# Kernel optimization log

Hardware: AMD Instinct MI355X
Metric: run time of the kernel (lower is better)

Reference implementation:

```python
import jax, jax.numpy as jnp
import numpy as np

D = 512          # input_size (feature dim)
C = 100          # num_classes
N = 2048         # test samples
ALPHA = 0.5      # regularization mixing parameter
SHRINK = 1e-4    # shrinkage_param


def setup_inputs() -> dict:
    key = jax.random.key(0)
    k1, k2, k3, k4, k5 = jax.random.split(key, 5)
    X = jax.random.normal(k1, (N, D), dtype=jnp.float32)
    muK = jax.random.normal(k2, (C, D), dtype=jnp.float32)
    # Per-class covariances: PSD, well-conditioned (like fitted streaming covariances)
    A = jax.random.normal(k3, (C, D, D), dtype=jnp.float32) * 0.05
    SigmaK = jnp.einsum('cij,ckj->cik', A, A) + 0.1 * jnp.eye(D, dtype=jnp.float32)
    B = jax.random.normal(k4, (D, D), dtype=jnp.float32) * 0.05
    Sigma = B @ B.T + 0.1 * jnp.eye(D, dtype=jnp.float32)
    # class counts (all > 0 so every class is active)
    cK = jax.random.uniform(k5, (C,), dtype=jnp.float32, minval=1.0, maxval=1000.0)
    return {"X": X, "muK": muK, "SigmaK": SigmaK, "Sigma": Sigma, "cK": cK}


def reference(X, muK, SigmaK, Sigma, cK):
    # RegSigmaK[k] = alpha * SigmaK[k] + (1-alpha) * Sigma           [C, D, D]
    RegSigmaK = ALPHA * SigmaK + (1.0 - ALPHA) * Sigma[None, :, :]
    # priors (classes with zero count get prior 1, then are masked to -inf below)
    s = jnp.sum(cK)
    prior = jnp.where(cK == 0, 1.0, cK / s)                          # [C]
    # Lambda[k] = pinv((1-sh) * RegSigmaK[k] + sh * I)               [C, D, D]
    eye = jnp.eye(D, dtype=RegSigmaK.dtype)
    Lambda = jnp.linalg.pinv((1.0 - SHRINK) * RegSigmaK + SHRINK * eye)
    # 0.5 * log ||RegSigmaK[k]||_F  (torch.norm default = Frobenius)
    half_lognorm = 0.5 * jnp.log(jnp.linalg.norm(RegSigmaK, axis=(1, 2)))  # [C]
    # batched Mahalanobis quadratic form: (x - mu_k)^T Lambda_k (x - mu_k)
    diff = X[:, None, :] - muK[None, :, :]                           # [N, C, D]
    quad = jnp.einsum('ncd,cde,nce->nc', diff, Lambda, diff)         # [N, C]
    scores = jnp.log(prior)[None, :] - half_lognorm[None, :] - 0.5 * quad
    scores = jnp.where((cK == 0)[None, :], -jnp.inf, scores)
    return scores
```

## Files before the change

kernel.cpp:

```cpp
#include <hip/hip_runtime.h>
#include <math.h>

#define DIM 512
#define NCLS 100
#define NS 2048
#define DD (DIM*DIM)
#define SHRINKV 1e-4f

typedef short bf16x8 __attribute__((ext_vector_type(8)));
typedef short s16x4 __attribute__((ext_vector_type(4)));
typedef float f32x4 __attribute__((ext_vector_type(4)));

static __device__ __forceinline__ short f2bf(float f) {
  unsigned int u = __float_as_uint(f);
  u += 0x7FFFu + ((u >> 16) & 1u);
  return (short)(u >> 16);
}

static __device__ __forceinline__ int xcd_swz(int bid, int nwg) {
  int xcd = bid & 7, idx = bid >> 3;
  int q = nwg >> 3, r = nwg & 7;
  return (xcd < r ? xcd * (q + 1) : r * (q + 1) + (xcd - r) * q) + idx;
}

__global__ __launch_bounds__(256) void prep_kernel(const float* __restrict__ SigmaK,
                                                   const float* __restrict__ Sigma,
                                                   float* __restrict__ M,
                                                   float* __restrict__ aux) {
  int b = blockIdx.x;
  int k = b >> 2, chunk = b & 3;
  const float* Sk = SigmaK + (size_t)k * DD;
  float* Mk = M + (size_t)k * DD;
  int base0 = chunk << 16;
  float fro = 0.f;
  const float oms = 1.0f - SHRINKV;
  for (int it = 0; it < 64; ++it) {
    int idx = base0 + (it << 10) + (threadIdx.x << 2);
    float4 a = *(const float4*)(Sk + idx);
    float4 g = *(const float4*)(Sigma + idx);
    int r = idx >> 9, c = idx & 511;
    float4 reg;
    reg.x = 0.5f*(a.x + g.x); reg.y = 0.5f*(a.y + g.y);
    reg.z = 0.5f*(a.z + g.z); reg.w = 0.5f*(a.w + g.w);
    fro += reg.x*reg.x + reg.y*reg.y + reg.z*reg.z + reg.w*reg.w;
    float4 m;
    m.x = oms*reg.x + ((r == c + 0) ? SHRINKV : 0.f);
    m.y = oms*reg.y + ((r == c + 1) ? SHRINKV : 0.f);
    m.z = oms*reg.z + ((r == c + 2) ? SHRINKV : 0.f);
    m.w = oms*reg.w + ((r == c + 3) ? SHRINKV : 0.f);
    *(float4*)(Mk + idx) = m;
  }
  __shared__ float red[4];
  int lane = threadIdx.x & 63, w = threadIdx.x >> 6;
  for (int o = 32; o > 0; o >>= 1) fro += __shfl_down(fro, o);
  if (lane == 0) red[w] = fro;
  __syncthreads();
  if (threadIdx.x == 0) atomicAdd(&aux[1 + k], red[0] + red[1] + red[2] + red[3]);
}

static __device__ __forceinline__ void fdiag_dev(float* __restrict__ Mk,
                                                 short* __restrict__ Wk,
                                                 int p0, int lane,
                                                 float* __restrict__ Llds) {
  float row[64];
  const float* src = Mk + (size_t)(p0 + lane) * DIM + p0;
  #pragma unroll
  for (int c4 = 0; c4 < 64; c4 += 4) {
    float4 v = *(const float4*)(src + c4);
    row[c4] = v.x; row[c4+1] = v.y; row[c4+2] = v.z; row[c4+3] = v.w;
  }
  #pragma unroll
  for (int j = 0; j < 64; ++j) {
    float diagv = __shfl(row[j], j);
    float dv = sqrtf(diagv);
    float rinv = 1.0f / dv;
    float myLj = row[j] * rinv;
    row[j] = myLj;
    #pragma unroll
    for (int c = j + 1; c < 64; ++c)
      row[c] = fmaf(-myLj, __shfl(myLj, c), row[c]);
  }
  #pragma unroll
  for (int c = 0; c < 64; ++c)
    Llds[lane * 68 + c] = (c <= lane) ? row[c] : 0.f;
  float w[64];
  #pragma unroll
  for (int r = 0; r < 64; ++r) {
    float s = 0.f;
    #pragma unroll
    for (int kk = 0; kk + 4 <= r; kk += 4) {
      float4 lv = *(const float4*)(Llds + r*68 + kk);
      s += lv.x*w[kk] + lv.y*w[kk+1] + lv.z*w[kk+2] + lv.w*w[kk+3];
    }
    #pragma unroll
    for (int kk = r & ~3; kk < r; ++kk) s += Llds[r*68 + kk] * w[kk];
    float rhs = ((r == lane) ? 1.0f : 0.0f) - s;
    w[r] = rhs / Llds[r*68 + r];
  }
  #pragma unroll
  for (int r = 0; r < 64; ++r) {
    Mk[(size_t)(p0 + r)*DIM + p0 + lane] = w[r];
    Wk[(size_t)(p0 + r)*DIM + p0 + lane] = f2bf(w[r]);
  }
}

__global__ __launch_bounds__(64) void fdiag_kernel(float* __restrict__ M,
                                                   short* __restrict__ Wb) {
  __shared__ float Llds[64 * 68];
  fdiag_dev(M + (size_t)blockIdx.x * DD, Wb + (size_t)blockIdx.x * DD,
            0, threadIdx.x, Llds);
}

__global__ __launch_bounds__(256) void trsm_kernel(float* __restrict__ M, int p) {
  __shared__ float TA[64 * 68];
  __shared__ float TB[64 * 68];
  int n = 7 - p;
  int wg = xcd_swz(blockIdx.x, NCLS * n);
  int cls = wg / n, bi = wg % n;
  int i = p + 1 + bi;
  float* Mk = M + (size_t)cls * DD;
  int tid = threadIdx.x;
  int ty = tid >> 4, tx = tid & 15;
  int sr = tid >> 2, sq = (tid & 3) << 4;
  int p0 = p << 6;
  {
    const float* a = Mk + (size_t)((i << 6) + sr)*DIM + p0 + sq;
    const float* b = Mk + (size_t)(p0 + sr)*DIM + p0 + sq;
    #pragma unroll
    for (int t4 = 0; t4 < 4; ++t4) {
      float4 va = *(const float4*)(a + 4*t4);
      TA[(sq+4*t4+0)*68+sr]=va.x; TA[(sq+4*t4+1)*68+sr]=va.y;
      TA[(sq+4*t4+2)*68+sr]=va.z; TA[(sq+4*t4+3)*68+sr]=va.w;
      float4 vb = *(const float4*)(b + 4*t4);
      TB[(sq+4*t4+0)*68+sr]=vb.x; TB[(sq+4*t4+1)*68+sr]=vb.y;
      TB[(sq+4*t4+2)*68+sr]=vb.z; TB[(sq+4*t4+3)*68+sr]=vb.w;
    }
  }
  __syncthreads();
  float acc[4][4];
  #pragma unroll
  for (int a2 = 0; a2 < 4; ++a2)
    #pragma unroll
    for (int b2 = 0; b2 < 4; ++b2) acc[a2][b2] = 0.f;
  #pragma unroll 16
  for (int m = 0; m < 64; ++m) {
    float4 av = *(const float4*)(TA + m*68 + (ty << 2));
    float4 bv = *(const float4*)(TB + m*68 + (tx << 2));
    float a4[4] = {av.x, av.y, av.z, av.w};
    float b4[4] = {bv.x, bv.y, bv.z, bv.w};
    #pragma unroll
    for (int ir = 0; ir < 4; ++ir)
      #pragma unroll
      for (int ic = 0; ic < 4; ++ic) acc[ir][ic] += a4[ir] * b4[ic];
  }
  #pragma unroll
  for (int q = 0; q < 4; ++q) {
    float4 v; v.x = acc[q][0]; v.y = acc[q][1]; v.z = acc[q][2]; v.w = acc[q][3];
    *(float4*)(Mk + (size_t)((i << 6) + (ty << 2) + q)*DIM + p0 + (tx << 2)) = v;
  }
  if (bi == 0) {
    __syncthreads();
    #pragma unroll
    for (int q = 0; q < 4; ++q)
      #pragma unroll
      for (int cc = 0; cc < 4; ++cc)
        TA[((tx << 2) + cc)*68 + (ty << 2) + q] = acc[q][cc];
    __syncthreads();
    float s2[4][4];
    #pragma unroll
    for (int a2 = 0; a2 < 4; ++a2)
      #pragma unroll
      for (int b2 = 0; b2 < 4; ++b2) s2[a2][b2] = 0.f;
    #pragma unroll 16
    for (int m = 0; m < 64; ++m) {
      float4 av = *(const float4*)(TA + m*68 + (ty << 2));
      float4 bv = *(const float4*)(TA + m*68 + (tx << 2));
      float a4[4] = {av.x, av.y, av.z, av.w};
      float b4[4] = {bv.x, bv.y, bv.z, bv.w};
      #pragma unroll
      for (int ir = 0; ir < 4; ++ir)
        #pragma unroll
        for (int ic = 0; ic < 4; ++ic) s2[ir][ic] += a4[ir] * b4[ic];
    }
    int d0 = (p + 1) << 6;
    #pragma unroll
    for (int q = 0; q < 4; ++q) {
      float* dst = Mk + (size_t)(d0 + (ty << 2) + q)*DIM + d0 + (tx << 2);
      float4 v = *(const float4*)dst;
      v.x -= s2[q][0]; v.y -= s2[q][1]; v.z -= s2[q][2]; v.w -= s2[q][3];
      *(float4*)dst = v;
    }
  }
}

__global__ __launch_bounds__(256) void combo_kernel(float* __restrict__ M,
                                                    short* __restrict__ Wb, int p) {
  __shared__ float TA[64 * 68];
  __shared__ float TB[64 * 68];
  int n = 7 - p;
  int T = n * (n + 1) / 2;
  int nsyrk = NCLS * (T - 1);
  int wg = xcd_swz(blockIdx.x, nsyrk + NCLS);
  int tid = threadIdx.x;
  if (wg >= nsyrk) {
    int cls = wg - nsyrk;
    if (tid < 64)
      fdiag_dev(M + (size_t)cls * DD, Wb + (size_t)cls * DD,
                (p + 1) << 6, tid, TA);
    return;
  }
  int cls = wg / (T - 1);
  int t = wg % (T - 1) + 1;
  int bi = 0;
  while (t > bi) { t -= bi + 1; ++bi; }
  int i = p + 1 + bi, j = p + 1 + t;
  float* Mk = M + (size_t)cls * DD;
  int ty = tid >> 4, tx = tid & 15;
  int sr = tid >> 2, sq = (tid & 3) << 4;
  {
    const float* a = Mk + (size_t)((i << 6) + sr)*DIM + (p << 6) + sq;
    const float* b = Mk + (size_t)((j << 6) + sr)*DIM + (p << 6) + sq;
    #pragma unroll
    for (int t4 = 0; t4 < 4; ++t4) {
      float4 va = *(const float4*)(a + 4*t4);
      TA[(sq+4*t4+0)*68+sr]=va.x; TA[(sq+4*t4+1)*68+sr]=va.y;
      TA[(sq+4*t4+2)*68+sr]=va.z; TA[(sq+4*t4+3)*68+sr]=va.w;
      float4 vb = *(const float4*)(b + 4*t4);
      TB[(sq+4*t4+0)*68+sr]=vb.x; TB[(sq+4*t4+1)*68+sr]=vb.y;
      TB[(sq+4*t4+2)*68+sr]=vb.z; TB[(sq+4*t4+3)*68+sr]=vb.w;
    }
  }
  __syncthreads();
  float acc[4][4];
  #pragma unroll
  for (int a = 0; a < 4; ++a)
    #pragma unroll
    for (int b = 0; b < 4; ++b) acc[a][b] = 0.f;
  #pragma unroll 16
  for (int m = 0; m < 64; ++m) {
    float4 av = *(const float4*)(TA + m*68 + (ty << 2));
    float4 bv = *(const float4*)(TB + m*68 + (tx << 2));
    float a4[4] = {av.x, av.y, av.z, av.w};
    float b4[4] = {bv.x, bv.y, bv.z, bv.w};
    #pragma unroll
    for (int ir = 0; ir < 4; ++ir)
      #pragma unroll
      for (int ic = 0; ic < 4; ++ic) acc[ir][ic] += a4[ir] * b4[ic];
  }
  #pragma unroll
  for (int q = 0; q < 4; ++q) {
    float* dst = Mk + (size_t)((i << 6) + (ty << 2) + q)*DIM + (j << 6) + (tx << 2);
    float4 v = *(const float4*)dst;
    v.x -= acc[q][0]; v.y -= acc[q][1]; v.z -= acc[q][2]; v.w -= acc[q][3];
    *(float4*)dst = v;
  }
}

__global__ __launch_bounds__(256) void colsweep_kernel(float* __restrict__ M,
                                                       short* __restrict__ Wb) {
  __shared__ float TL[2][64 * 68];
  __shared__ float TW[2][64 * 68];
  int wg = xcd_swz(blockIdx.x, NCLS * 7);
  int cls = wg / 7;
  int j = wg % 7;
  float* Mk = M + (size_t)cls * DD;
  short* Wk = Wb + (size_t)cls * DD;
  int tid = threadIdx.x;
  int ty = tid >> 4, tx = tid & 15;
  int sr = tid >> 2, sq = (tid & 3) << 4;
  for (int i = j + 1; i < 8; ++i) {
    auto stageLW = [&](int k, int buf) {
      const float* a = Mk + (size_t)((i << 6) + sr)*DIM + (k << 6) + sq;
      const float* b = Mk + (size_t)((j << 6) + sr)*DIM + (k << 6) + sq;
      #pragma unroll
      for (int t4 = 0; t4 < 4; ++t4) {
        float4 va = *(const float4*)(a + 4*t4);
        TL[buf][(sq+4*t4+0)*68+sr]=va.x; TL[buf][(sq+4*t4+1)*68+sr]=va.y;
        TL[buf][(sq+4*t4+2)*68+sr]=va.z; TL[buf][(sq+4*t4+3)*68+sr]=va.w;
        *(float4*)(TW[buf] + sr*68 + sq + 4*t4) = *(const float4*)(b + 4*t4);
      }
    };
    float acc[4][4];
    #pragma unroll
    for (int a = 0; a < 4; ++a)
      #pragma unroll
      for (int b = 0; b < 4; ++b) acc[a][b] = 0.f;
    stageLW(j, 0);
    __syncthreads();
    int cur = 0;
    for (int k = j; k < i; ++k) {
      if (k + 1 < i) stageLW(k + 1, cur ^ 1);
      #pragma unroll 16
      for (int m = 0; m < 64; ++m) {
        float4 av = *(const float4*)(TL[cur] + m*68 + (ty << 2));
        float4 bv = *(const float4*)(TW[cur] + m*68 + (tx << 2));
        float a4[4] = {av.x, av.y, av.z, av.w};
        float b4[4] = {bv.x, bv.y, bv.z, bv.w};
        #pragma unroll
        for (int ir = 0; ir < 4; ++ir)
          #pragma unroll
          for (int ic = 0; ic < 4; ++ic) acc[ir][ic] += a4[ir] * b4[ic];
      }
      __syncthreads();
      cur ^= 1;
    }
    #pragma unroll
    for (int q = 0; q < 4; ++q) {
      float4 v; v.x = acc[q][0]; v.y = acc[q][1]; v.z = acc[q][2]; v.w = acc[q][3];
      *(float4*)(TW[0] + ((ty << 2) + q)*68 + (tx << 2)) = v;
    }
    {
      const float* a = Mk + (size_t)((i << 6) + sr)*DIM + (i << 6) + sq;
      #pragma unroll
      for (int t4 = 0; t4 < 4; ++t4) {
        float4 va = *(const float4*)(a + 4*t4);
        TL[0][(sq+4*t4+0)*68+sr]=va.x; TL[0][(sq+4*t4+1)*68+sr]=va.y;
        TL[0][(sq+4*t4+2)*68+sr]=va.z; TL[0][(sq+4*t4+3)*68+sr]=va.w;
      }
    }
    __syncthreads();
    float r2[4][4];
    #pragma unroll
    for (int a = 0; a < 4; ++a)
      #pragma unroll
      for (int b = 0; b < 4; ++b) r2[a][b] = 0.f;
    #pragma unroll 16
    for (int m = 0; m < 64; ++m) {
      float4 av = *(const float4*)(TL[0] + m*68 + (ty << 2));
      float4 bv = *(const float4*)(TW[0] + m*68 + (tx << 2));
      float a4[4] = {av.x, av.y, av.z, av.w};
      float b4[4] = {bv.x, bv.y, bv.z, bv.w};
      #pragma unroll
      for (int ir = 0; ir < 4; ++ir)
        #pragma unroll
        for (int ic = 0; ic < 4; ++ic) r2[ir][ic] += a4[ir] * b4[ic];
    }
    #pragma unroll
    for (int q = 0; q < 4; ++q) {
      int a = (ty << 2) + q;
      float4 v; v.x = -r2[q][0]; v.y = -r2[q][1]; v.z = -r2[q][2]; v.w = -r2[q][3];
      *(float4*)(Mk + (size_t)((j << 6) + a)*DIM + (i << 6) + (tx << 2)) = v;
      s16x4 h;
      h[0] = f2bf(v.x); h[1] = f2bf(v.y); h[2] = f2bf(v.z); h[3] = f2bf(v.w);
      *(s16x4*)(Wk + (size_t)((i << 6) + a)*DIM + (j << 6) + (tx << 2)) = h;
    }
    __syncthreads();
  }
}

__global__ __launch_bounds__(256) void score_kernel(const float* __restrict__ X,
                                                    const float* __restrict__ muK,
                                                    const float* __restrict__ cK,
                                                    const short* __restrict__ W,
                                                    const float* __restrict__ aux,
                                                    float* __restrict__ out) {
  __shared__ __align__(16) char WB4[4][8192];
  __shared__ float sred[4];
  int bid = blockIdx.x;
  int wg = ((bid & 7) * 400) + (bid >> 3);
  int kc = wg >> 5;
  int n0 = (wg & 31) << 6;
  int tid = threadIdx.x;
  int lane = tid & 63, wv = tid >> 6;
  const short* Wk = W + (size_t)kc * DD;
  const float* mu = muK + (size_t)kc * DIM;
  int r16 = lane & 15;
  int k8 = (lane >> 4) << 3;
  int arow = (wv << 4) + r16;

  int lrow = lane >> 3;
  int lcolel = ((lane & 7) ^ lrow) << 3;

  constexpr int SJT[36] = {0,1,1, 2,3,2,3,2,3,3, 4,5,4,5,4,5,4,5,4,5,5,
                           6,7,6,7,6,7,6,7,6,7,6,7,6,7,7};
  constexpr int SDC[36] = {0,0,1, 0,0,1,1,2,2,3, 0,0,1,1,2,2,3,3,4,4,5,
                           0,0,1,1,2,2,3,3,4,4,5,5,6,6,7};

  bf16x8 af[8][2];
  #pragma unroll
  for (int dc = 0; dc < 8; ++dc) {
    #pragma unroll
    for (int ks = 0; ks < 2; ++ks) {
      int col = (dc << 6) + (ks << 5) + k8;
      const float* xp = X + (size_t)(n0 + arow)*DIM + col;
      float4 x0 = *(const float4*)xp;
      float4 x1 = *(const float4*)(xp + 4);
      float4 m0 = *(const float4*)(mu + col);
      float4 m1 = *(const float4*)(mu + col + 4);
      bf16x8 h;
      h[0]=f2bf(x0.x-m0.x); h[1]=f2bf(x0.y-m0.y); h[2]=f2bf(x0.z-m0.z); h[3]=f2bf(x0.w-m0.w);
      h[4]=f2bf(x1.x-m1.x); h[5]=f2bf(x1.y-m1.y); h[6]=f2bf(x1.z-m1.z); h[7]=f2bf(x1.w-m1.w);
      af[dc][ks] = h;
    }
  }

  auto issue = [&](int s) {
    const int b = s & 3;
    const int rbase = SJT[s] << 6;
    const int cc = (SDC[s] << 6) + lcolel;
    #pragma unroll
    for (int q = 0; q < 2; ++q) {
      const short* g = Wk + (size_t)(rbase + (q << 5) + (wv << 3) + lrow)*DIM + cc;
      __builtin_amdgcn_global_load_lds(
          (const __attribute__((address_space(1))) void*)g,
          (__attribute__((address_space(3))) void*)(WB4[b] + (q << 12) + (wv << 10)),
          16, 0, 0);
    }
  };

  float qp[4] = {0.f, 0.f, 0.f, 0.f};
  f32x4 acc[2][4];
  #pragma unroll
  for (int a = 0; a < 2; ++a)
    #pragma unroll
    for (int jj = 0; jj < 4; ++jj) { acc[a][jj][0]=0.f; acc[a][jj][1]=0.f; acc[a][jj][2]=0.f; acc[a][jj][3]=0.f; }

  issue(0);
  issue(1);
  #pragma unroll
  for (int s = 0; s < 36; ++s) {
    const int jt = SJT[s], dc = SDC[s];
    if (s + 2 < 36) issue(s + 2);
    if (s < 34)      asm volatile("s_waitcnt vmcnt(4)" ::: "memory");
    else if (s == 34) asm volatile("s_waitcnt vmcnt(2)" ::: "memory");
    else              asm volatile("s_waitcnt vmcnt(0)" ::: "memory");
    __builtin_amdgcn_s_barrier();
    __builtin_amdgcn_sched_barrier(0);
    __builtin_amdgcn_s_setprio(1);
    #pragma unroll
    for (int ks = 0; ks < 2; ++ks) {
      #pragma unroll
      for (int jj = 0; jj < 4; ++jj) {
        int brow = (jj << 4) + r16;
        bf16x8 bfr = *(const bf16x8*)((const char*)WB4[s & 3] +
                     (((brow << 7) + (((ks << 5) + k8) << 1)) ^ ((brow & 7) << 4)));
        acc[jt & 1][jj] = __builtin_amdgcn_mfma_f32_16x16x32_bf16(af[dc][ks], bfr, acc[jt & 1][jj], 0, 0, 0);
      }
    }
    __builtin_amdgcn_s_setprio(0);
    if (s == 2 || s == 9 || s == 20 || s == 35) {
      #pragma unroll
      for (int a = 0; a < 2; ++a)
        #pragma unroll
        for (int jj = 0; jj < 4; ++jj)
          #pragma unroll
          for (int r = 0; r < 4; ++r) {
            float y = acc[a][jj][r]; qp[r] += y * y;
            acc[a][jj][r] = 0.f;
          }
    }
  }
  #pragma unroll
  for (int r = 0; r < 4; ++r) {
    qp[r] += __shfl_xor(qp[r], 1);
    qp[r] += __shfl_xor(qp[r], 2);
    qp[r] += __shfl_xor(qp[r], 4);
    qp[r] += __shfl_xor(qp[r], 8);
  }
  {
    float v = (tid < NCLS) ? cK[tid] : 0.f;
    #pragma unroll
    for (int o = 32; o > 0; o >>= 1) v += __shfl_xor(v, o);
    if (lane == 0) sred[wv] = v;
  }
  __syncthreads();
  float sumck = sred[0] + sred[1] + sred[2] + sred[3];
  float ck = cK[kc];
  float base;
  if (ck == 0.f) base = -INFINITY;
  else base = logf(ck) - logf(sumck) - 0.25f * logf(aux[1 + kc]);
  if ((lane & 15) == 0) {
    int nbase = n0 + (wv << 4) + ((lane >> 4) << 2);
    #pragma unroll
    for (int r = 0; r < 4; ++r)
      out[(size_t)(nbase + r)*NCLS + kc] = base - 0.5f * qp[r];
  }
}

extern "C" void kernel_launch(void* const* d_in, const int* in_sizes, int n_in,
                              void* d_out, int out_size, void* d_ws, size_t ws_size,
                              hipStream_t stream) {
  (void)in_sizes; (void)n_in; (void)out_size; (void)ws_size;
  const float* X      = (const float*)d_in[0];
  const float* muK    = (const float*)d_in[1];
  const float* SigmaK = (const float*)d_in[2];
  const float* Sigma  = (const float*)d_in[3];
  const float* cK     = (const float*)d_in[4];
  float* out = (float*)d_out;
  char* ws = (char*)d_ws;
  float* M   = (float*)ws;
  short* W   = (short*)(ws + (size_t)NCLS * DD * 4);
  float* aux = (float*)(ws + (size_t)NCLS * DD * 6);

  hipMemsetAsync(aux, 0, (1 + NCLS) * sizeof(float), stream);
  prep_kernel<<<400, 256, 0, stream>>>(SigmaK, Sigma, M, aux);
  fdiag_kernel<<<NCLS, 64, 0, stream>>>(M, W);
  for (int p = 0; p < 7; ++p) {
    int n = 7 - p;
    int T = n * (n + 1) / 2;
    trsm_kernel<<<NCLS * n, 256, 0, stream>>>(M, p);
    combo_kernel<<<NCLS * (T - 1) + NCLS, 256, 0, stream>>>(M, W, p);
  }
  colsweep_kernel<<<NCLS * 7, 256, 0, stream>>>(M, W);
  score_kernel<<<NCLS * 32, 256, 0, stream>>>(X, muK, cK, W, aux, out);
}
```

Measured before the change: 798.5 us.

## Interleave inverse column sweep into blocked Cholesky panel steps

The separate column-sweep kernel that formed the triangular inverse after the factorization is removed. Its work is spread across the eight panel steps: each panel kernel now also computes the inverse block row for the just-finished panel, and the diagonal-block factorization is folded into the first TRSM workgroup rather than run as extra workgroups in the SYRK kernel. The aim is to drop one long serial kernel with deep per-workgroup loops and fill the small late panel launches with independent work. In exchange the diagonal factor runs serially at the end of one workgroup, which lengthens the critical path of each step.

```diff
diff --git a/kernel.cpp b/kernel.cpp
--- a/kernel.cpp
+++ b/kernel.cpp
@@ -111,21 +111,193 @@
             0, threadIdx.x, Llds);
 }
 
-__global__ __launch_bounds__(256) void trsm_kernel(float* __restrict__ M, int p) {
+__global__ __launch_bounds__(256) void panelA_kernel(float* __restrict__ M,
+                                                     short* __restrict__ Wb, int p) {
+  __shared__ float SA[2][64 * 68];
+  __shared__ float SB[2][64 * 68];
+  int n = 7 - p;
+  int nwg = n + p;
+  int wg = xcd_swz(blockIdx.x, NCLS * nwg);
+  int cls = wg / nwg, r = wg % nwg;
+  float* Mk = M + (size_t)cls * DD;
+  short* Wk = Wb + (size_t)cls * DD;
+  int tid = threadIdx.x;
+  int ty = tid >> 4, tx = tid & 15;
+  int sr = tid >> 2, sq = (tid & 3) << 4;
+  int p0 = p << 6;
+
+  if (r < n) {
+    int i = p + 1 + r;
+    {
+      const float* a = Mk + (size_t)((i << 6) + sr)*DIM + p0 + sq;
+      const float* b = Mk + (size_t)(p0 + sr)*DIM + p0 + sq;
+      #pragma unroll
+      for (int t4 = 0; t4 < 4; ++t4) {
+        float4 va = *(const float4*)(a + 4*t4);
+        SA[0][(sq+4*t4+0)*68+sr]=va.x; SA[0][(sq+4*t4+1)*68+sr]=va.y;
+        SA[0][(sq+4*t4+2)*68+sr]=va.z; SA[0][(sq+4*t4+3)*68+sr]=va.w;
+        float4 vb = *(const float4*)(b + 4*t4);
+        SA[1][(sq+4*t4+0)*68+sr]=vb.x; SA[1][(sq+4*t4+1)*68+sr]=vb.y;
+        SA[1][(sq+4*t4+2)*68+sr]=vb.z; SA[1][(sq+4*t4+3)*68+sr]=vb.w;
+      }
+    }
+    __syncthreads();
+    float acc[4][4];
+    #pragma unroll
+    for (int a2 = 0; a2 < 4; ++a2)
+      #pragma unroll
+      for (int b2 = 0; b2 < 4; ++b2) acc[a2][b2] = 0.f;
+    #pragma unroll 16
+    for (int m = 0; m < 64; ++m) {
+      float4 av = *(const float4*)(&SA[0][m*68 + (ty << 2)]);
+      float4 bv = *(const float4*)(&SA[1][m*68 + (tx << 2)]);
+      float a4[4] = {av.x, av.y, av.z, av.w};
+      float b4[4] = {bv.x, bv.y, bv.z, bv.w};
+      #pragma unroll
+      for (int ir = 0; ir < 4; ++ir)
+        #pragma unroll
+        for (int ic = 0; ic < 4; ++ic) acc[ir][ic] += a4[ir] * b4[ic];
+    }
+    #pragma unroll
+    for (int q = 0; q < 4; ++q) {
+      float4 v; v.x = acc[q][0]; v.y = acc[q][1]; v.z = acc[q][2]; v.w = acc[q][3];
+      *(float4*)(Mk + (size_t)((i << 6) + (ty << 2) + q)*DIM + p0 + (tx << 2)) = v;
+    }
+    if (r == 0) {
+      __syncthreads();
+      #pragma unroll
+      for (int q = 0; q < 4; ++q)
+        #pragma unroll
+        for (int cc = 0; cc < 4; ++cc)
+          SA[0][((tx << 2) + cc)*68 + (ty << 2) + q] = acc[q][cc];
+      __syncthreads();
+      float s2[4][4];
+      #pragma unroll
+      for (int a2 = 0; a2 < 4; ++a2)
+        #pragma unroll
+        for (int b2 = 0; b2 < 4; ++b2) s2[a2][b2] = 0.f;
+      #pragma unroll 16
+      for (int m = 0; m < 64; ++m) {
+        float4 av = *(const float4*)(&SA[0][m*68 + (ty << 2)]);
+        float4 bv = *(const float4*)(&SA[0][m*68 + (tx << 2)]);
+        float a4[4] = {av.x, av.y, av.z, av.w};
+        float b4[4] = {bv.x, bv.y, bv.z, bv.w};
+        #pragma unroll
+        for (int ir = 0; ir < 4; ++ir)
+          #pragma unroll
+          for (int ic = 0; ic < 4; ++ic) s2[ir][ic] += a4[ir] * b4[ic];
+      }
+      int d0 = (p + 1) << 6;
+      #pragma unroll
+      for (int q = 0; q < 4; ++q) {
+        float* dst = Mk + (size_t)(d0 + (ty << 2) + q)*DIM + d0 + (tx << 2);
+        float4 v = *(const float4*)dst;
+        v.x -= s2[q][0]; v.y -= s2[q][1]; v.z -= s2[q][2]; v.w -= s2[q][3];
+        *(float4*)dst = v;
+      }
+      __syncthreads();
+      if (tid < 64)
+        fdiag_dev(Mk, Wk, d0, tid, SA[1]);
+    }
+  } else {
+    int j = r - n;
+    auto stageLW = [&](int k, int buf) {
+      const float* a = Mk + (size_t)(p0 + sr)*DIM + (k << 6) + sq;
+      const float* b = Mk + (size_t)((j << 6) + sr)*DIM + (k << 6) + sq;
+      #pragma unroll
+      for (int t4 = 0; t4 < 4; ++t4) {
+        float4 va = *(const float4*)(a + 4*t4);
+        SA[buf][(sq+4*t4+0)*68+sr]=va.x; SA[buf][(sq+4*t4+1)*68+sr]=va.y;
+        SA[buf][(sq+4*t4+2)*68+sr]=va.z; SA[buf][(sq+4*t4+3)*68+sr]=va.w;
+        *(float4*)(&SB[buf][sr*68 + sq + 4*t4]) = *(const float4*)(b + 4*t4);
+      }
+    };
+    float acc[4][4];
+    #pragma unroll
+    for (int a = 0; a < 4; ++a)
+      #pragma unroll
+      for (int b = 0; b < 4; ++b) acc[a][b] = 0.f;
+    stageLW(j, 0);
+    __syncthreads();
+    int cur = 0;
+    for (int k = j; k < p; ++k) {
+      if (k + 1 < p) stageLW(k + 1, cur ^ 1);
+      #pragma unroll 16
+      for (int m = 0; m < 64; ++m) {
+        float4 av = *(const float4*)(&SA[cur][m*68 + (ty << 2)]);
+        float4 bv = *(const float4*)(&SB[cur][m*68 + (tx << 2)]);
+        float a4[4] = {av.x, av.y, av.z, av.w};
+        float b4[4] = {bv.x, bv.y, bv.z, bv.w};
+        #pragma unroll
+        for (int ir = 0; ir < 4; ++ir)
+          #pragma unroll
+          for (int ic = 0; ic < 4; ++ic) acc[ir][ic] += a4[ir] * b4[ic];
+      }
+      __syncthreads();
+      cur ^= 1;
+    }
+    #pragma unroll
+    for (int q = 0; q < 4; ++q) {
+      float4 v; v.x = acc[q][0]; v.y = acc[q][1]; v.z = acc[q][2]; v.w = acc[q][3];
+      *(float4*)(&SB[0][((ty << 2) + q)*68 + (tx << 2)]) = v;
+    }
+    {
+      const float* a = Mk + (size_t)(p0 + sr)*DIM + p0 + sq;
+      #pragma unroll
+      for (int t4 = 0; t4 < 4; ++t4) {
+        float4 va = *(const float4*)(a + 4*t4);
+        SA[0][(sq+4*t4+0)*68+sr]=va.x; SA[0][(sq+4*t4+1)*68+sr]=va.y;
+        SA[0][(sq+4*t4+2)*68+sr]=va.z; SA[0][(sq+4*t4+3)*68+sr]=va.w;
+      }
+    }
+    __syncthreads();
+    float r2[4][4];
+    #pragma unroll
+    for (int a = 0; a < 4; ++a)
+      #pragma unroll
+      for (int b = 0; b < 4; ++b) r2[a][b] = 0.f;
+    #pragma unroll 16
+    for (int m = 0; m < 64; ++m) {
+      float4 av = *(const float4*)(&SA[0][m*68 + (ty << 2)]);
+      float4 bv = *(const float4*)(&SB[0][m*68 + (tx << 2)]);
+      float a4[4] = {av.x, av.y, av.z, av.w};
+      float b4[4] = {bv.x, bv.y, bv.z, bv.w};
+      #pragma unroll
+      for (int ir = 0; ir < 4; ++ir)
+        #pragma unroll
+        for (int ic = 0; ic < 4; ++ic) r2[ir][ic] += a4[ir] * b4[ic];
+    }
+    #pragma unroll
+    for (int q = 0; q < 4; ++q) {
+      int a = (ty << 2) + q;
+      float4 v; v.x = -r2[q][0]; v.y = -r2[q][1]; v.z = -r2[q][2]; v.w = -r2[q][3];
+      *(float4*)(Mk + (size_t)((j << 6) + a)*DIM + p0 + (tx << 2)) = v;
+      s16x4 h;
+      h[0] = f2bf(v.x); h[1] = f2bf(v.y); h[2] = f2bf(v.z); h[3] = f2bf(v.w);
+      *(s16x4*)(Wk + (size_t)(p0 + a)*DIM + (j << 6) + (tx << 2)) = h;
+    }
+  }
+}
+
+__global__ __launch_bounds__(256) void panelB_kernel(float* __restrict__ M, int p) {
   __shared__ float TA[64 * 68];
   __shared__ float TB[64 * 68];
   int n = 7 - p;
-  int wg = xcd_swz(blockIdx.x, NCLS * n);
-  int cls = wg / n, bi = wg % n;
-  int i = p + 1 + bi;
+  int T = n * (n + 1) / 2;
+  int nwg = NCLS * (T - 1);
+  int wg = xcd_swz(blockIdx.x, nwg);
+  int cls = wg / (T - 1);
+  int t = wg % (T - 1) + 1;
+  int bi = 0;
+  while (t > bi) { t -= bi + 1; ++bi; }
+  int i = p + 1 + bi, j = p + 1 + t;
   float* Mk = M + (size_t)cls * DD;
   int tid = threadIdx.x;
   int ty = tid >> 4, tx = tid & 15;
   int sr = tid >> 2, sq = (tid & 3) << 4;
-  int p0 = p << 6;
   {
-    const float* a = Mk + (size_t)((i << 6) + sr)*DIM + p0 + sq;
-    const float* b = Mk + (size_t)(p0 + sr)*DIM + p0 + sq;
+    const float* a = Mk + (size_t)((i << 6) + sr)*DIM + (p << 6) + sq;
+    const float* b = Mk + (size_t)((j << 6) + sr)*DIM + (p << 6) + sq;
     #pragma unroll
     for (int t4 = 0; t4 < 4; ++t4) {
       float4 va = *(const float4*)(a + 4*t4);
@@ -139,100 +311,6 @@
   __syncthreads();
   float acc[4][4];
   #pragma unroll
-  for (int a2 = 0; a2 < 4; ++a2)
-    #pragma unroll
-    for (int b2 = 0; b2 < 4; ++b2) acc[a2][b2] = 0.f;
-  #pragma unroll 16
-  for (int m = 0; m < 64; ++m) {
-    float4 av = *(const float4*)(TA + m*68 + (ty << 2));
-    float4 bv = *(const float4*)(TB + m*68 + (tx << 2));
-    float a4[4] = {av.x, av.y, av.z, av.w};
-    float b4[4] = {bv.x, bv.y, bv.z, bv.w};
-    #pragma unroll
-    for (int ir = 0; ir < 4; ++ir)
-      #pragma unroll
-      for (int ic = 0; ic < 4; ++ic) acc[ir][ic] += a4[ir] * b4[ic];
-  }
-  #pragma unroll
-  for (int q = 0; q < 4; ++q) {
-    float4 v; v.x = acc[q][0]; v.y = acc[q][1]; v.z = acc[q][2]; v.w = acc[q][3];
-    *(float4*)(Mk + (size_t)((i << 6) + (ty << 2) + q)*DIM + p0 + (tx << 2)) = v;
-  }
-  if (bi == 0) {
-    __syncthreads();
-    #pragma unroll
-    for (int q = 0; q < 4; ++q)
-      #pragma unroll
-      for (int cc = 0; cc < 4; ++cc)
-        TA[((tx << 2) + cc)*68 + (ty << 2) + q] = acc[q][cc];
-    __syncthreads();
-    float s2[4][4];
-    #pragma unroll
-    for (int a2 = 0; a2 < 4; ++a2)
-      #pragma unroll
-      for (int b2 = 0; b2 < 4; ++b2) s2[a2][b2] = 0.f;
-    #pragma unroll 16
-    for (int m = 0; m < 64; ++m) {
-      float4 av = *(const float4*)(TA + m*68 + (ty << 2));
-      float4 bv = *(const float4*)(TA + m*68 + (tx << 2));
-      float a4[4] = {av.x, av.y, av.z, av.w};
-      float b4[4] = {bv.x, bv.y, bv.z, bv.w};
-      #pragma unroll
-      for (int ir = 0; ir < 4; ++ir)
-        #pragma unroll
-        for (int ic = 0; ic < 4; ++ic) s2[ir][ic] += a4[ir] * b4[ic];
-    }
-    int d0 = (p + 1) << 6;
-    #pragma unroll
-    for (int q = 0; q < 4; ++q) {
-      float* dst = Mk + (size_t)(d0 + (ty << 2) + q)*DIM + d0 + (tx << 2);
-      float4 v = *(const float4*)dst;
-      v.x -= s2[q][0]; v.y -= s2[q][1]; v.z -= s2[q][2]; v.w -= s2[q][3];
-      *(float4*)dst = v;
-    }
-  }
-}
-
-__global__ __launch_bounds__(256) void combo_kernel(float* __restrict__ M,
-                                                    short* __restrict__ Wb, int p) {
-  __shared__ float TA[64 * 68];
-  __shared__ float TB[64 * 68];
-  int n = 7 - p;
-  int T = n * (n + 1) / 2;
-  int nsyrk = NCLS * (T - 1);
-  int wg = xcd_swz(blockIdx.x, nsyrk + NCLS);
-  int tid = threadIdx.x;
-  if (wg >= nsyrk) {
-    int cls = wg - nsyrk;
-    if (tid < 64)
-      fdiag_dev(M + (size_t)cls * DD, Wb + (size_t)cls * DD,
-                (p + 1) << 6, tid, TA);
-    return;
-  }
-  int cls = wg / (T - 1);
-  int t = wg % (T - 1) + 1;
-  int bi = 0;
-  while (t > bi) { t -= bi + 1; ++bi; }
-  int i = p + 1 + bi, j = p + 1 + t;
-  float* Mk = M + (size_t)cls * DD;
-  int ty = tid >> 4, tx = tid & 15;
-  int sr = tid >> 2, sq = (tid & 3) << 4;
-  {
-    const float* a = Mk + (size_t)((i << 6) + sr)*DIM + (p << 6) + sq;
-    const float* b = Mk + (size_t)((j << 6) + sr)*DIM + (p << 6) + sq;
-    #pragma unroll
-    for (int t4 = 0; t4 < 4; ++t4) {
-      float4 va = *(const float4*)(a + 4*t4);
-      TA[(sq+4*t4+0)*68+sr]=va.x; TA[(sq+4*t4+1)*68+sr]=va.y;
-      TA[(sq+4*t4+2)*68+sr]=va.z; TA[(sq+4*t4+3)*68+sr]=va.w;
-      float4 vb = *(const float4*)(b + 4*t4);
-      TB[(sq+4*t4+0)*68+sr]=vb.x; TB[(sq+4*t4+1)*68+sr]=vb.y;
-      TB[(sq+4*t4+2)*68+sr]=vb.z; TB[(sq+4*t4+3)*68+sr]=vb.w;
-    }
-  }
-  __syncthreads();
-  float acc[4][4];
-  #pragma unroll
   for (int a = 0; a < 4; ++a)
     #pragma unroll
     for (int b = 0; b < 4; ++b) acc[a][b] = 0.f;
@@ -253,98 +331,6 @@
     float4 v = *(const float4*)dst;
     v.x -= acc[q][0]; v.y -= acc[q][1]; v.z -= acc[q][2]; v.w -= acc[q][3];
     *(float4*)dst = v;
-  }
-}
-
-__global__ __launch_bounds__(256) void colsweep_kernel(float* __restrict__ M,
-                                                       short* __restrict__ Wb) {
-  __shared__ float TL[2][64 * 68];
-  __shared__ float TW[2][64 * 68];
-  int wg = xcd_swz(blockIdx.x, NCLS * 7);
-  int cls = wg / 7;
-  int j = wg % 7;
-  float* Mk = M + (size_t)cls * DD;
-  short* Wk = Wb + (size_t)cls * DD;
-  int tid = threadIdx.x;
-  int ty = tid >> 4, tx = tid & 15;
-  int sr = tid >> 2, sq = (tid & 3) << 4;
-  for (int i = j + 1; i < 8; ++i) {
-    auto stageLW = [&](int k, int buf) {
-      const float* a = Mk + (size_t)((i << 6) + sr)*DIM + (k << 6) + sq;
-      const float* b = Mk + (size_t)((j << 6) + sr)*DIM + (k << 6) + sq;
-      #pragma unroll
-      for (int t4 = 0; t4 < 4; ++t4) {
-        float4 va = *(const float4*)(a + 4*t4);
-        TL[buf][(sq+4*t4+0)*68+sr]=va.x; TL[buf][(sq+4*t4+1)*68+sr]=va.y;
-        TL[buf][(sq+4*t4+2)*68+sr]=va.z; TL[buf][(sq+4*t4+3)*68+sr]=va.w;
-        *(float4*)(TW[buf] + sr*68 + sq + 4*t4) = *(const float4*)(b + 4*t4);
-      }
-    };
-    float acc[4][4];
-    #pragma unroll
-    for (int a = 0; a < 4; ++a)
-      #pragma unroll
-      for (int b = 0; b < 4; ++b) acc[a][b] = 0.f;
-    stageLW(j, 0);
-    __syncthreads();
-    int cur = 0;
-    for (int k = j; k < i; ++k) {
-      if (k + 1 < i) stageLW(k + 1, cur ^ 1);
-      #pragma unroll 16
-      for (int m = 0; m < 64; ++m) {
-        float4 av = *(const float4*)(TL[cur] + m*68 + (ty << 2));
-        float4 bv = *(const float4*)(TW[cur] + m*68 + (tx << 2));
-        float a4[4] = {av.x, av.y, av.z, av.w};
-        float b4[4] = {bv.x, bv.y, bv.z, bv.w};
-        #pragma unroll
-        for (int ir = 0; ir < 4; ++ir)
-          #pragma unroll
-          for (int ic = 0; ic < 4; ++ic) acc[ir][ic] += a4[ir] * b4[ic];
-      }
-      __syncthreads();
-      cur ^= 1;
-    }
-    #pragma unroll
-    for (int q = 0; q < 4; ++q) {
-      float4 v; v.x = acc[q][0]; v.y = acc[q][1]; v.z = acc[q][2]; v.w = acc[q][3];
-      *(float4*)(TW[0] + ((ty << 2) + q)*68 + (tx << 2)) = v;
-    }
-    {
-      const float* a = Mk + (size_t)((i << 6) + sr)*DIM + (i << 6) + sq;
-      #pragma unroll
-      for (int t4 = 0; t4 < 4; ++t4) {
-        float4 va = *(const float4*)(a + 4*t4);
-        TL[0][(sq+4*t4+0)*68+sr]=va.x; TL[0][(sq+4*t4+1)*68+sr]=va.y;
-        TL[0][(sq+4*t4+2)*68+sr]=va.z; TL[0][(sq+4*t4+3)*68+sr]=va.w;
-      }
-    }
-    __syncthreads();
-    float r2[4][4];
-    #pragma unroll
-    for (int a = 0; a < 4; ++a)
-      #pragma unroll
-      for (int b = 0; b < 4; ++b) r2[a][b] = 0.f;
-    #pragma unroll 16
-    for (int m = 0; m < 64; ++m) {
-      float4 av = *(const float4*)(TL[0] + m*68 + (ty << 2));
-      float4 bv = *(const float4*)(TW[0] + m*68 + (tx << 2));
-      float a4[4] = {av.x, av.y, av.z, av.w};
-      float b4[4] = {bv.x, bv.y, bv.z, bv.w};
-      #pragma unroll
-      for (int ir = 0; ir < 4; ++ir)
-        #pragma unroll
-        for (int ic = 0; ic < 4; ++ic) r2[ir][ic] += a4[ir] * b4[ic];
-    }
-    #pragma unroll
-    for (int q = 0; q < 4; ++q) {
-      int a = (ty << 2) + q;
-      float4 v; v.x = -r2[q][0]; v.y = -r2[q][1]; v.z = -r2[q][2]; v.w = -r2[q][3];
-      *(float4*)(Mk + (size_t)((j << 6) + a)*DIM + (i << 6) + (tx << 2)) = v;
-      s16x4 h;
-      h[0] = f2bf(v.x); h[1] = f2bf(v.y); h[2] = f2bf(v.z); h[3] = f2bf(v.w);
-      *(s16x4*)(Wk + (size_t)((i << 6) + a)*DIM + (j << 6) + (tx << 2)) = h;
-    }
-    __syncthreads();
   }
 }
 
@@ -492,15 +478,15 @@
   short* W   = (short*)(ws + (size_t)NCLS * DD * 4);
   float* aux = (float*)(ws + (size_t)NCLS * DD * 6);
 
-  hipMemsetAsync(aux, 0, (1 + NCLS) * sizeof(float), stream);
+  (void)hipMemsetAsync(aux, 0, (1 + NCLS) * sizeof(float), stream);
   prep_kernel<<<400, 256, 0, stream>>>(SigmaK, Sigma, M, aux);
   fdiag_kernel<<<NCLS, 64, 0, stream>>>(M, W);
-  for (int p = 0; p < 7; ++p) {
+  for (int p = 0; p < 8; ++p) {
     int n = 7 - p;
-    int T = n * (n + 1) / 2;
-    trsm_kernel<<<NCLS * n, 256, 0, stream>>>(M, p);
-    combo_kernel<<<NCLS * (T - 1) + NCLS, 256, 0, stream>>>(M, W, p);
-  }
-  colsweep_kernel<<<NCLS * 7, 256, 0, stream>>>(M, W);
+    int nwg = n + p;
+    panelA_kernel<<<NCLS * nwg, 256, 0, stream>>>(M, W, p);
+    int Tm1 = n * (n + 1) / 2 - 1;
+    if (Tm1 > 0) panelB_kernel<<<NCLS * Tm1, 256, 0, stream>>>(M, p);
+  }
   score_kernel<<<NCLS * 32, 256, 0, stream>>>(X, muK, cK, W, aux, out);
 }
```

Measured after the change: 827.6 us. 3.6% more time.
